# Performance work log

Hardware: AMD Instinct MI355X
Metric: run time of the kernel (lower is better)

## Reference

```python
import jax, jax.numpy as jnp
import numpy as np

EPS = 1e-12  # matches torch F.normalize default eps

def _l2_normalize(x):
    # torch.nn.functional.normalize: x / max(||x||_2, eps)
    n = jnp.sqrt(jnp.sum(x * x, axis=-1, keepdims=True))
    return x / jnp.maximum(n, EPS)

def setup_inputs() -> dict:
    key = jax.random.key(0)
    kq, kk, kv = jax.random.split(key, 3)
    B, N, M, C = 8, 4096, 4096, 256
    return {
        "query": jax.random.normal(kq, (B, N, C), dtype=jnp.float32),
        "key": jax.random.normal(kk, (B, M, C), dtype=jnp.float32),
        "value": jax.random.normal(kv, (B, M, C), dtype=jnp.float32),
    }

def reference(query, key, value):
    B, N, C = query.shape
    q = _l2_normalize(query)          # (B, N, C)
    k = _l2_normalize(key)            # (B, M, C)
    kv = jnp.einsum('bmc,bmd->bcd', k, value)   # (B, C, C)
    context = jnp.einsum('bnc,bcd->bnd', q, kv) # (B, N, C)
    return context / N
```

## Files before the change

### kernel.cpp

```cpp
#include <hip/hip_runtime.h>

typedef __attribute__((ext_vector_type(4))) float v4f;
typedef __attribute__((ext_vector_type(8))) short short8;
typedef unsigned short u16;
typedef unsigned int u32;
typedef __attribute__((ext_vector_type(2))) unsigned int u32x2;
typedef __attribute__((ext_vector_type(4))) unsigned short u16x4;
typedef __attribute__((ext_vector_type(8))) unsigned short u16x8;

#define CDIM 256
#define NB 8
#define NN 4096
#define MM 4096

static __device__ __forceinline__ u16 f2bf(float f) {
  unsigned u = __float_as_uint(f);
  u = (u + 0x7fffu + ((u >> 16) & 1u)) >> 16;
  return (u16)u;
}
static __device__ __forceinline__ float bf2f(u16 h) {
  return __uint_as_float(((unsigned)h) << 16);
}
static __device__ __forceinline__ u32 pack2(float a, float b) {
  return (u32)f2bf(a) | ((u32)f2bf(b) << 16);
}

static __device__ __forceinline__ u32x2 xpose4(u32 A, u32 B, int hi) {
  u32 tA = (u32)__shfl_xor((int)A, 32);
  u32 tB = (u32)__shfl_xor((int)B, 32);
  u32 U = (hi < 2) ? A : tB;
  u32 V = (hi < 2) ? tA : B;
  u32 tU = (u32)__shfl_xor((int)U, 16);
  u32 tV = (u32)__shfl_xor((int)V, 16);
  u32 Up, Vp;
  if ((hi & 1) == 0) {
    Up = (U & 0xffffu) | (tU << 16);
    Vp = (V & 0xffffu) | (tV << 16);
  } else {
    Up = (tU >> 16) | (U & 0xffff0000u);
    Vp = (tV >> 16) | (V & 0xffff0000u);
  }
  return (u32x2){Up, Vp};
}

__global__ __launch_bounds__(512) void kv_kernel(const float* __restrict__ key,
                                                 const float* __restrict__ value,
                                                 u16* __restrict__ partial, int KC) {
  __shared__ __align__(16) u16 knT[2][256 * 64];
  __shared__ __align__(16) u16 vT[2][256 * 64];
  int t = threadIdx.x;
  int b = blockIdx.y, s = blockIdx.x;
  int w = t >> 6, lane = t & 63, lo = lane & 15, hi = lane >> 4;

  const float* kbase = key + ((size_t)b * MM + (size_t)s * KC) * CDIM;
  const float* vbase = value + ((size_t)b * MM + (size_t)s * KC) * CDIM;

  v4f acc[2][16];
  #pragma unroll
  for (int i = 0; i < 2; i++)
    #pragma unroll
    for (int d = 0; d < 16; d++) acc[i][d] = (v4f){0.f, 0.f, 0.f, 0.f};

  v4f kq[4], vq[4];

  auto LOADS = [&](int sc, int it) {
    int row = sc * 64 + w * 8 + it * 4 + hi;
    const float* kr = kbase + (size_t)row * CDIM + lo * 4;
    const float* vr = vbase + (size_t)row * CDIM + lo * 4;
    #pragma unroll
    for (int qt = 0; qt < 4; ++qt) {
      kq[qt] = *(const v4f*)(kr + qt * 64);
      vq[qt] = *(const v4f*)(vr + qt * 64);
    }
  };
  auto STORE = [&](int bufi, int it) {
    int m0 = w * 8 + it * 4;
    float ss = 0.f;
    #pragma unroll
    for (int qt = 0; qt < 4; ++qt)
      ss += kq[qt][0]*kq[qt][0] + kq[qt][1]*kq[qt][1] + kq[qt][2]*kq[qt][2] + kq[qt][3]*kq[qt][3];
    #pragma unroll
    for (int m = 1; m < 16; m <<= 1) ss += __shfl_xor(ss, m);
    float sc_ = 1.0f / fmaxf(sqrtf(ss), 1e-12f);
    #pragma unroll
    for (int qt = 0; qt < 4; ++qt) {
      int c = qt * 64 + lo * 4 + hi;
      int idx = (c * 64 + m0) ^ ((c & 7) << 3);
      u32x2 ko = xpose4(pack2(kq[qt][0] * sc_, kq[qt][1] * sc_),
                        pack2(kq[qt][2] * sc_, kq[qt][3] * sc_), hi);
      *(u32x2*)&knT[bufi][idx] = ko;
      u32x2 vo = xpose4(pack2(vq[qt][0], vq[qt][1]),
                        pack2(vq[qt][2], vq[qt][3]), hi);
      *(u32x2*)&vT[bufi][idx] = vo;
    }
  };
  auto MF = [&](const u16* KB, const u16* VB) {
    #pragma unroll
    for (int kk = 0; kk < 64; kk += 32) {
      int acol = kk + hi * 8;
      int r0 = w * 32 + lo, r1 = w * 32 + 16 + lo;
      short8 a0 = *(const short8*)&KB[(r0 * 64 + acol) ^ ((r0 & 7) << 3)];
      short8 a1 = *(const short8*)&KB[(r1 * 64 + acol) ^ ((r1 & 7) << 3)];
      #pragma unroll
      for (int dt = 0; dt < 16; ++dt) {
        int drow = dt * 16 + lo;
        short8 bb = *(const short8*)&VB[(drow * 64 + acol) ^ ((drow & 7) << 3)];
        acc[0][dt] = __builtin_amdgcn_mfma_f32_16x16x32_bf16(bb, a0, acc[0][dt], 0, 0, 0);
        acc[1][dt] = __builtin_amdgcn_mfma_f32_16x16x32_bf16(bb, a1, acc[1][dt], 0, 0, 0);
      }
    }
  };

  int nsc = KC >> 6;
  LOADS(0, 0); STORE(0, 0);
  LOADS(0, 1); STORE(0, 1);
  __syncthreads();
  for (int sc = 0; sc < nsc; ++sc) {
    int nb = (sc + 1) & 1;
    if (sc + 1 < nsc) LOADS(sc + 1, 0);
    MF(knT[sc & 1], vT[sc & 1]);
    if (sc + 1 < nsc) {
      STORE(nb, 0);
      LOADS(sc + 1, 1);
      STORE(nb, 1);
    }
    __syncthreads();
  }

  size_t base = ((size_t)(s * NB + b)) << 16;
  #pragma unroll
  for (int i = 0; i < 2; i++) {
    int cc = w * 32 + i * 16 + lo;
    #pragma unroll
    for (int dt = 0; dt < 16; ++dt) {
      int dd = dt * 16 + hi * 4;
      #pragma unroll
      for (int r = 0; r < 4; r++)
        partial[base + (size_t)(dd + r) * 256 + cc] = f2bf(acc[i][dt][r]);
    }
  }
}

__global__ __launch_bounds__(256) void red_kernel(const u16* __restrict__ partial,
                                                  u16* __restrict__ kvT, int splits) {
  int j = blockIdx.x * 256 + threadIdx.x;
  int b = j >> 13;
  int e0 = (j & 8191) * 8;
  size_t off = ((size_t)b << 16) + e0;
  const float inv = 1.0f / 4096.0f;
  float sum[8] = {0.f, 0.f, 0.f, 0.f, 0.f, 0.f, 0.f, 0.f};
  for (int s = 0; s < splits; ++s) {
    u16x8 p = *(const u16x8*)&partial[(((size_t)s * NB) << 16) + off];
    #pragma unroll
    for (int x = 0; x < 8; ++x) sum[x] += bf2f(p[x]);
  }
  u16x8 o;
  #pragma unroll
  for (int x = 0; x < 8; ++x) o[x] = f2bf(sum[x] * inv);
  *(u16x8*)&kvT[off] = o;
}

__global__ __launch_bounds__(512) void ctx_kernel(const float* __restrict__ query,
                                                  const u16* __restrict__ kvT,
                                                  float* __restrict__ out) {
  __shared__ __align__(16) u16 qn[2][16 * 256];
  int t = threadIdx.x;
  int b = blockIdx.y;
  int tile0 = blockIdx.x * 4;
  int w = t >> 6, lane = t & 63, lo = lane & 15, hi = lane >> 4;
  int row = t >> 5, l32 = t & 31;
  const float* qbase = query + (size_t)b * NN * CDIM + (size_t)row * CDIM + l32 * 8;

  const float* qr0 = qbase + (size_t)(tile0 * 16) * CDIM;
  v4f x0 = *(const v4f*)qr0;
  v4f x1 = *(const v4f*)(qr0 + 4);

  const u16* kvb = kvT + ((size_t)b << 16);
  short8 Bf[2][8];
  #pragma unroll
  for (int i = 0; i < 2; i++) {
    int dr = (2 * w + i) * 16 + lo;
    #pragma unroll
    for (int kc = 0; kc < 8; kc++)
      Bf[i][kc] = *(const short8*)&kvb[(size_t)dr * 256 + kc * 32 + 8 * hi];
  }

  {
    float ss = x0[0]*x0[0] + x0[1]*x0[1] + x0[2]*x0[2] + x0[3]*x0[3]
             + x1[0]*x1[0] + x1[1]*x1[1] + x1[2]*x1[2] + x1[3]*x1[3];
    #pragma unroll
    for (int m = 1; m < 32; m <<= 1) ss += __shfl_xor(ss, m);
    float sc = 1.0f / fmaxf(sqrtf(ss), 1e-12f);
    u16x8 qb;
    qb[0] = f2bf(x0[0] * sc); qb[1] = f2bf(x0[1] * sc);
    qb[2] = f2bf(x0[2] * sc); qb[3] = f2bf(x0[3] * sc);
    qb[4] = f2bf(x1[0] * sc); qb[5] = f2bf(x1[1] * sc);
    qb[6] = f2bf(x1[2] * sc); qb[7] = f2bf(x1[3] * sc);
    *(u16x8*)&qn[0][(row * 256 + l32 * 8) ^ ((row & 7) << 3)] = qb;
  }

  int cur = 0;
  #pragma unroll
  for (int nt = 0; nt < 4; ++nt) {
    v4f p0, p1;
    if (nt < 3) {
      const float* qr = qbase + (size_t)((tile0 + nt + 1) * 16) * CDIM;
      p0 = *(const v4f*)qr;
      p1 = *(const v4f*)(qr + 4);
    }
    __syncthreads();
    short8 Af[8];
    #pragma unroll
    for (int kc = 0; kc < 8; kc++)
      Af[kc] = *(const short8*)&qn[cur][(lo * 256 + kc * 32 + 8 * hi) ^ ((lo & 7) << 3)];
    v4f acc0 = (v4f){0.f, 0.f, 0.f, 0.f};
    v4f acc1 = (v4f){0.f, 0.f, 0.f, 0.f};
    #pragma unroll
    for (int kc = 0; kc < 8; kc++) {
      acc0 = __builtin_amdgcn_mfma_f32_16x16x32_bf16(Af[kc], Bf[0][kc], acc0, 0, 0, 0);
      acc1 = __builtin_amdgcn_mfma_f32_16x16x32_bf16(Af[kc], Bf[1][kc], acc1, 0, 0, 0);
    }
    int n0 = (tile0 + nt) * 16;
    #pragma unroll
    for (int r = 0; r < 4; r++) {
      size_t ro = (size_t)(b * NN + n0 + 4 * hi + r) * CDIM;
      out[ro + (2 * w) * 16 + lo] = acc0[r];
      out[ro + (2 * w + 1) * 16 + lo] = acc1[r];
    }
    if (nt < 3) {
      float ss = p0[0]*p0[0] + p0[1]*p0[1] + p0[2]*p0[2] + p0[3]*p0[3]
               + p1[0]*p1[0] + p1[1]*p1[1] + p1[2]*p1[2] + p1[3]*p1[3];
      #pragma unroll
      for (int m = 1; m < 32; m <<= 1) ss += __shfl_xor(ss, m);
      float sc = 1.0f / fmaxf(sqrtf(ss), 1e-12f);
      u16x8 qb;
      qb[0] = f2bf(p0[0] * sc); qb[1] = f2bf(p0[1] * sc);
      qb[2] = f2bf(p0[2] * sc); qb[3] = f2bf(p0[3] * sc);
      qb[4] = f2bf(p1[0] * sc); qb[5] = f2bf(p1[1] * sc);
      qb[6] = f2bf(p1[2] * sc); qb[7] = f2bf(p1[3] * sc);
      *(u16x8*)&qn[cur ^ 1][(row * 256 + l32 * 8) ^ ((row & 7) << 3)] = qb;
      cur ^= 1;
    }
  }
}

extern "C" void kernel_launch(void* const* d_in, const int* in_sizes, int n_in,
                              void* d_out, int out_size, void* d_ws, size_t ws_size,
                              hipStream_t stream) {
  const float* q = (const float*)d_in[0];
  const float* k = (const float*)d_in[1];
  const float* v = (const float*)d_in[2];
  float* out = (float*)d_out;

  int splits = 32;
  while (splits > 2) {
    size_t need = ((size_t)splits + 1ull) * 1048576ull;
    if (need <= ws_size) break;
    splits >>= 1;
  }
  u16* partial = (u16*)d_ws;
  u16* kvT = (u16*)((char*)d_ws + (size_t)splits * 1048576ull);

  kv_kernel<<<dim3(splits, NB), dim3(512), 0, stream>>>(k, v, partial, MM / splits);
  red_kernel<<<dim3(256), dim3(256), 0, stream>>>(partial, kvT, splits);
  ctx_kernel<<<dim3(64, NB), dim3(512), 0, stream>>>(q, kvT, out);
}
```

Measured before the change: 56.83 us.

## Double kv_kernel block to 1024 threads and stage partial writes through LDS

The kv_kernel block grows to 16 waves, and work is split over the output d dimension, so each wave holds half the accumulators and loads one 4-row slice per stage instead of two. This raises the number of waves available to hide latency and cuts register pressure per wave. The epilogue now transposes the bf16 accumulators through shared memory in two halves and writes partials with coalesced 16-byte stores, replacing scattered 2-byte global stores. The cost is extra barriers and LDS traffic in the epilogue, and with 64KB of LDS per block occupancy may still be limited.

```diff
diff --git a/kernel.cpp b/kernel.cpp
--- a/kernel.cpp
+++ b/kernel.cpp
@@ -43,28 +43,29 @@
   return (u32x2){Up, Vp};
 }
 
-__global__ __launch_bounds__(512) void kv_kernel(const float* __restrict__ key,
-                                                 const float* __restrict__ value,
-                                                 u16* __restrict__ partial, int KC) {
+__global__ __launch_bounds__(1024, 4) void kv_kernel(const float* __restrict__ key,
+                                                     const float* __restrict__ value,
+                                                     u16* __restrict__ partial, int KC) {
   __shared__ __align__(16) u16 knT[2][256 * 64];
   __shared__ __align__(16) u16 vT[2][256 * 64];
   int t = threadIdx.x;
   int b = blockIdx.y, s = blockIdx.x;
   int w = t >> 6, lane = t & 63, lo = lane & 15, hi = lane >> 4;
+  int wc = w & 7, wd = w >> 3;
 
   const float* kbase = key + ((size_t)b * MM + (size_t)s * KC) * CDIM;
   const float* vbase = value + ((size_t)b * MM + (size_t)s * KC) * CDIM;
 
-  v4f acc[2][16];
+  v4f acc[2][8];
   #pragma unroll
   for (int i = 0; i < 2; i++)
     #pragma unroll
-    for (int d = 0; d < 16; d++) acc[i][d] = (v4f){0.f, 0.f, 0.f, 0.f};
+    for (int d = 0; d < 8; d++) acc[i][d] = (v4f){0.f, 0.f, 0.f, 0.f};
 
   v4f kq[4], vq[4];
 
-  auto LOADS = [&](int sc, int it) {
-    int row = sc * 64 + w * 8 + it * 4 + hi;
+  auto LOADS = [&](int sc) {
+    int row = sc * 64 + w * 4 + hi;
     const float* kr = kbase + (size_t)row * CDIM + lo * 4;
     const float* vr = vbase + (size_t)row * CDIM + lo * 4;
     #pragma unroll
@@ -73,8 +74,8 @@
       vq[qt] = *(const v4f*)(vr + qt * 64);
     }
   };
-  auto STORE = [&](int bufi, int it) {
-    int m0 = w * 8 + it * 4;
+  auto STORE = [&](int bufi) {
+    int m0 = w * 4;
     float ss = 0.f;
     #pragma unroll
     for (int qt = 0; qt < 4; ++qt)
@@ -98,12 +99,12 @@
     #pragma unroll
     for (int kk = 0; kk < 64; kk += 32) {
       int acol = kk + hi * 8;
-      int r0 = w * 32 + lo, r1 = w * 32 + 16 + lo;
+      int r0 = wc * 32 + lo, r1 = wc * 32 + 16 + lo;
       short8 a0 = *(const short8*)&KB[(r0 * 64 + acol) ^ ((r0 & 7) << 3)];
       short8 a1 = *(const short8*)&KB[(r1 * 64 + acol) ^ ((r1 & 7) << 3)];
       #pragma unroll
-      for (int dt = 0; dt < 16; ++dt) {
-        int drow = dt * 16 + lo;
+      for (int dt = 0; dt < 8; ++dt) {
+        int drow = (wd * 8 + dt) * 16 + lo;
         short8 bb = *(const short8*)&VB[(drow * 64 + acol) ^ ((drow & 7) << 3)];
         acc[0][dt] = __builtin_amdgcn_mfma_f32_16x16x32_bf16(bb, a0, acc[0][dt], 0, 0, 0);
         acc[1][dt] = __builtin_amdgcn_mfma_f32_16x16x32_bf16(bb, a1, acc[1][dt], 0, 0, 0);
@@ -112,31 +113,39 @@
   };
 
   int nsc = KC >> 6;
-  LOADS(0, 0); STORE(0, 0);
-  LOADS(0, 1); STORE(0, 1);
+  LOADS(0);
+  STORE(0);
   __syncthreads();
   for (int sc = 0; sc < nsc; ++sc) {
-    int nb = (sc + 1) & 1;
-    if (sc + 1 < nsc) LOADS(sc + 1, 0);
+    if (sc + 1 < nsc) LOADS(sc + 1);
     MF(knT[sc & 1], vT[sc & 1]);
-    if (sc + 1 < nsc) {
-      STORE(nb, 0);
-      LOADS(sc + 1, 1);
-      STORE(nb, 1);
-    }
+    if (sc + 1 < nsc) STORE((sc + 1) & 1);
     __syncthreads();
   }
 
-  size_t base = ((size_t)(s * NB + b)) << 16;
-  #pragma unroll
-  for (int i = 0; i < 2; i++) {
-    int cc = w * 32 + i * 16 + lo;
-    #pragma unroll
-    for (int dt = 0; dt < 16; ++dt) {
-      int dd = dt * 16 + hi * 4;
+  u16* S = &knT[0][0];
+  size_t pbase = ((size_t)(s * NB + b)) << 16;
+  #pragma unroll
+  for (int p = 0; p < 2; ++p) {
+    if (p) __syncthreads();
+    if (wd == p) {
       #pragma unroll
-      for (int r = 0; r < 4; r++)
-        partial[base + (size_t)(dd + r) * 256 + cc] = f2bf(acc[i][dt][r]);
+      for (int i = 0; i < 2; i++) {
+        int c = wc * 32 + i * 16 + lo;
+        #pragma unroll
+        for (int dt = 0; dt < 8; ++dt) {
+          int dl = dt * 16 + hi * 4;
+          #pragma unroll
+          for (int r = 0; r < 4; r++)
+            S[(dl + r) * 256 + c] = f2bf(acc[i][dt][r]);
+        }
+      }
+    }
+    __syncthreads();
+    #pragma unroll
+    for (int j = 0; j < 4; ++j) {
+      int f = j * 8192 + t * 8;
+      *(u16x8*)&partial[pbase + (size_t)p * 32768 + f] = *(const u16x8*)&S[f];
     }
   }
 }
@@ -261,7 +270,7 @@
   u16* partial = (u16*)d_ws;
   u16* kvT = (u16*)((char*)d_ws + (size_t)splits * 1048576ull);
 
-  kv_kernel<<<dim3(splits, NB), dim3(512), 0, stream>>>(k, v, partial, MM / splits);
+  kv_kernel<<<dim3(splits, NB), dim3(1024), 0, stream>>>(k, v, partial, MM / splits);
   red_kernel<<<dim3(256), dim3(256), 0, stream>>>(partial, kvT, splits);
   ctx_kernel<<<dim3(64, NB), dim3(512), 0, stream>>>(q, kvT, out);
 }
```

Result: slower. 65.48 us (+15.2%).

## Shrink kv staging chunks and double-buffer register prefetch with lighter barriers

Applied to the files above, without the earlier changes.

The kv_kernel now stages 32-row chunks instead of 64 in a half-size LDS double buffer, with a new swizzle for the 32-column layout. Two register sets (A/B) let the global loads for the chunk after next be issued while the MFMAs on the current chunk run. The main loop is unrolled by two and uses one custom barrier per chunk: an explicit LDS wait, s_barrier and a scheduling fence. The aim is to hide global load latency better and cut barrier and LDS cost, at the price of more live registers, which may cause spills under the 512-thread launch bound.

```diff
diff --git a/kernel.cpp b/kernel.cpp
--- a/kernel.cpp
+++ b/kernel.cpp
@@ -23,6 +23,10 @@
 }
 static __device__ __forceinline__ u32 pack2(float a, float b) {
   return (u32)f2bf(a) | ((u32)f2bf(b) << 16);
+}
+
+static __device__ __forceinline__ int sidx32(int c, int m) {
+  return (c * 32 + m) ^ (((c >> 1) & 7) << 3);
 }
 
 static __device__ __forceinline__ u32x2 xpose4(u32 A, u32 B, int hi) {
@@ -43,11 +47,17 @@
   return (u32x2){Up, Vp};
 }
 
+#define BARRIER() do { \
+  asm volatile("s_waitcnt lgkmcnt(0)" ::: "memory"); \
+  __builtin_amdgcn_s_barrier(); \
+  __builtin_amdgcn_sched_barrier(0); \
+} while (0)
+
 __global__ __launch_bounds__(512) void kv_kernel(const float* __restrict__ key,
                                                  const float* __restrict__ value,
                                                  u16* __restrict__ partial, int KC) {
-  __shared__ __align__(16) u16 knT[2][256 * 64];
-  __shared__ __align__(16) u16 vT[2][256 * 64];
+  __shared__ __align__(16) u16 KL[2][256 * 32];
+  __shared__ __align__(16) u16 VL[2][256 * 32];
   int t = threadIdx.x;
   int b = blockIdx.y, s = blockIdx.x;
   int w = t >> 6, lane = t & 63, lo = lane & 15, hi = lane >> 4;
@@ -61,10 +71,10 @@
     #pragma unroll
     for (int d = 0; d < 16; d++) acc[i][d] = (v4f){0.f, 0.f, 0.f, 0.f};
 
-  v4f kq[4], vq[4];
-
-  auto LOADS = [&](int sc, int it) {
-    int row = sc * 64 + w * 8 + it * 4 + hi;
+  v4f kqA[4], vqA[4], kqB[4], vqB[4];
+
+  auto LOADS = [&](int sc, v4f (&kq)[4], v4f (&vq)[4]) {
+    int row = sc * 32 + w * 4 + hi;
     const float* kr = kbase + (size_t)row * CDIM + lo * 4;
     const float* vr = vbase + (size_t)row * CDIM + lo * 4;
     #pragma unroll
@@ -73,8 +83,8 @@
       vq[qt] = *(const v4f*)(vr + qt * 64);
     }
   };
-  auto STORE = [&](int bufi, int it) {
-    int m0 = w * 8 + it * 4;
+  auto STORE = [&](int bufi, v4f (&kq)[4], v4f (&vq)[4]) {
+    int m0 = w * 4;
     float ss = 0.f;
     #pragma unroll
     for (int qt = 0; qt < 4; ++qt)
@@ -85,46 +95,48 @@
     #pragma unroll
     for (int qt = 0; qt < 4; ++qt) {
       int c = qt * 64 + lo * 4 + hi;
-      int idx = (c * 64 + m0) ^ ((c & 7) << 3);
+      int idx = sidx32(c, m0);
       u32x2 ko = xpose4(pack2(kq[qt][0] * sc_, kq[qt][1] * sc_),
                         pack2(kq[qt][2] * sc_, kq[qt][3] * sc_), hi);
-      *(u32x2*)&knT[bufi][idx] = ko;
+      *(u32x2*)&KL[bufi][idx] = ko;
       u32x2 vo = xpose4(pack2(vq[qt][0], vq[qt][1]),
                         pack2(vq[qt][2], vq[qt][3]), hi);
-      *(u32x2*)&vT[bufi][idx] = vo;
+      *(u32x2*)&VL[bufi][idx] = vo;
     }
   };
   auto MF = [&](const u16* KB, const u16* VB) {
-    #pragma unroll
-    for (int kk = 0; kk < 64; kk += 32) {
-      int acol = kk + hi * 8;
-      int r0 = w * 32 + lo, r1 = w * 32 + 16 + lo;
-      short8 a0 = *(const short8*)&KB[(r0 * 64 + acol) ^ ((r0 & 7) << 3)];
-      short8 a1 = *(const short8*)&KB[(r1 * 64 + acol) ^ ((r1 & 7) << 3)];
-      #pragma unroll
-      for (int dt = 0; dt < 16; ++dt) {
-        int drow = dt * 16 + lo;
-        short8 bb = *(const short8*)&VB[(drow * 64 + acol) ^ ((drow & 7) << 3)];
-        acc[0][dt] = __builtin_amdgcn_mfma_f32_16x16x32_bf16(bb, a0, acc[0][dt], 0, 0, 0);
-        acc[1][dt] = __builtin_amdgcn_mfma_f32_16x16x32_bf16(bb, a1, acc[1][dt], 0, 0, 0);
+    int acol = hi * 8;
+    int r0 = w * 32 + lo, r1 = w * 32 + 16 + lo;
+    short8 a0 = *(const short8*)&KB[sidx32(r0, 0) ^ 0 ? sidx32(r0, 0) : sidx32(r0, 0)];
+    a0 = *(const short8*)&KB[(r0 * 32 + acol) ^ (((r0 >> 1) & 7) << 3)];
+    short8 a1 = *(const short8*)&KB[(r1 * 32 + acol) ^ (((r1 >> 1) & 7) << 3)];
+    #pragma unroll
+    for (int dt = 0; dt < 16; ++dt) {
+      int drow = dt * 16 + lo;
+      short8 bb = *(const short8*)&VB[(drow * 32 + acol) ^ (((drow >> 1) & 7) << 3)];
+      acc[0][dt] = __builtin_amdgcn_mfma_f32_16x16x32_bf16(bb, a0, acc[0][dt], 0, 0, 0);
+      acc[1][dt] = __builtin_amdgcn_mfma_f32_16x16x32_bf16(bb, a1, acc[1][dt], 0, 0, 0);
+    }
+  };
+
+  int nsc = KC >> 5;
+  LOADS(0, kqA, vqA);
+  LOADS(1, kqB, vqB);
+  STORE(0, kqA, vqA);
+  BARRIER();
+  for (int i = 0; i < nsc; i += 2) {
+    if (i + 2 < nsc) LOADS(i + 2, kqA, vqA);
+    MF(KL[0], VL[0]);
+    if (i + 1 < nsc) {
+      STORE(1, kqB, vqB);
+      BARRIER();
+      if (i + 3 < nsc) LOADS(i + 3, kqB, vqB);
+      MF(KL[1], VL[1]);
+      if (i + 2 < nsc) {
+        STORE(0, kqA, vqA);
+        BARRIER();
       }
     }
-  };
-
-  int nsc = KC >> 6;
-  LOADS(0, 0); STORE(0, 0);
-  LOADS(0, 1); STORE(0, 1);
-  __syncthreads();
-  for (int sc = 0; sc < nsc; ++sc) {
-    int nb = (sc + 1) & 1;
-    if (sc + 1 < nsc) LOADS(sc + 1, 0);
-    MF(knT[sc & 1], vT[sc & 1]);
-    if (sc + 1 < nsc) {
-      STORE(nb, 0);
-      LOADS(sc + 1, 1);
-      STORE(nb, 1);
-    }
-    __syncthreads();
   }
 
   size_t base = ((size_t)(s * NB + b)) << 16;
```

After: 57.78 us. No clear change (+1.7%).

## Split K/V normalize-transpose into separate pre-pass writing bf16 swizzled panels

Applied to the files above, without the earlier changes.

Moves K normalization, bf16 conversion and transposition out of the KV GEMM into a new conv_kernel that writes pre-swizzled 32-row bf16 panels to workspace. The GEMM kernel then copies those panels straight into shared memory and runs MFMAs on 32-wide K chunks with double buffering. This aims to take the conversion and shuffle work off the GEMM's critical path. In exchange it adds an extra launch and a round trip of bf16 panels through global memory.

```diff
diff --git a/kernel.cpp b/kernel.cpp
--- a/kernel.cpp
+++ b/kernel.cpp
@@ -5,13 +5,13 @@
 typedef unsigned short u16;
 typedef unsigned int u32;
 typedef __attribute__((ext_vector_type(2))) unsigned int u32x2;
-typedef __attribute__((ext_vector_type(4))) unsigned short u16x4;
 typedef __attribute__((ext_vector_type(8))) unsigned short u16x8;
 
 #define CDIM 256
 #define NB 8
 #define NN 4096
 #define MM 4096
+#define PANEL 8192
 
 static __device__ __forceinline__ u16 f2bf(float f) {
   unsigned u = __float_as_uint(f);
@@ -23,6 +23,10 @@
 }
 static __device__ __forceinline__ u32 pack2(float a, float b) {
   return (u32)f2bf(a) | ((u32)f2bf(b) << 16);
+}
+
+static __device__ __forceinline__ int sidx32(int c, int m) {
+  return (c * 32 + m) ^ (((c >> 1) & 7) << 3);
 }
 
 static __device__ __forceinline__ u32x2 xpose4(u32 A, u32 B, int hi) {
@@ -43,17 +47,53 @@
   return (u32x2){Up, Vp};
 }
 
-__global__ __launch_bounds__(512) void kv_kernel(const float* __restrict__ key,
-                                                 const float* __restrict__ value,
-                                                 u16* __restrict__ partial, int KC) {
-  __shared__ __align__(16) u16 knT[2][256 * 64];
-  __shared__ __align__(16) u16 vT[2][256 * 64];
+__global__ __launch_bounds__(512) void conv_kernel(const float* __restrict__ key,
+                                                   const float* __restrict__ value,
+                                                   u16* __restrict__ ktp,
+                                                   u16* __restrict__ vtp) {
+  int t = threadIdx.x;
+  int w = t >> 6, lane = t & 63, lo = lane & 15, hi = lane >> 4;
+  int m0 = w * 4;
+  size_t grow = (size_t)blockIdx.x * 32 + m0 + hi;
+  const float* kr = key + grow * CDIM + lo * 4;
+  const float* vr = value + grow * CDIM + lo * 4;
+  v4f kq[4], vq[4];
+  #pragma unroll
+  for (int qt = 0; qt < 4; ++qt) {
+    kq[qt] = *(const v4f*)(kr + qt * 64);
+    vq[qt] = *(const v4f*)(vr + qt * 64);
+  }
+  float ss = 0.f;
+  #pragma unroll
+  for (int qt = 0; qt < 4; ++qt)
+    ss += kq[qt][0]*kq[qt][0] + kq[qt][1]*kq[qt][1] + kq[qt][2]*kq[qt][2] + kq[qt][3]*kq[qt][3];
+  #pragma unroll
+  for (int m = 1; m < 16; m <<= 1) ss += __shfl_xor(ss, m);
+  float sc_ = 1.0f / fmaxf(sqrtf(ss), 1e-12f);
+  u16* kp = ktp + (size_t)blockIdx.x * PANEL;
+  u16* vp = vtp + (size_t)blockIdx.x * PANEL;
+  #pragma unroll
+  for (int qt = 0; qt < 4; ++qt) {
+    int c = qt * 64 + lo * 4 + hi;
+    int idx = sidx32(c, m0);
+    u32x2 ko = xpose4(pack2(kq[qt][0] * sc_, kq[qt][1] * sc_),
+                      pack2(kq[qt][2] * sc_, kq[qt][3] * sc_), hi);
+    *(u32x2*)&kp[idx] = ko;
+    u32x2 vo = xpose4(pack2(vq[qt][0], vq[qt][1]),
+                      pack2(vq[qt][2], vq[qt][3]), hi);
+    *(u32x2*)&vp[idx] = vo;
+  }
+}
+
+__global__ __launch_bounds__(512) void gemm_kernel(const u16* __restrict__ ktp,
+                                                   const u16* __restrict__ vtp,
+                                                   u16* __restrict__ partial, int KC) {
+  __shared__ __align__(16) u16 KL[2][PANEL];
+  __shared__ __align__(16) u16 VL[2][PANEL];
   int t = threadIdx.x;
   int b = blockIdx.y, s = blockIdx.x;
   int w = t >> 6, lane = t & 63, lo = lane & 15, hi = lane >> 4;
-
-  const float* kbase = key + ((size_t)b * MM + (size_t)s * KC) * CDIM;
-  const float* vbase = value + ((size_t)b * MM + (size_t)s * KC) * CDIM;
+  size_t p0 = ((size_t)b * MM + (size_t)s * KC) >> 5;
 
   v4f acc[2][16];
   #pragma unroll
@@ -61,68 +101,50 @@
     #pragma unroll
     for (int d = 0; d < 16; d++) acc[i][d] = (v4f){0.f, 0.f, 0.f, 0.f};
 
-  v4f kq[4], vq[4];
-
-  auto LOADS = [&](int sc, int it) {
-    int row = sc * 64 + w * 8 + it * 4 + hi;
-    const float* kr = kbase + (size_t)row * CDIM + lo * 4;
-    const float* vr = vbase + (size_t)row * CDIM + lo * 4;
-    #pragma unroll
-    for (int qt = 0; qt < 4; ++qt) {
-      kq[qt] = *(const v4f*)(kr + qt * 64);
-      vq[qt] = *(const v4f*)(vr + qt * 64);
+  int soff = t * 16;
+
+  auto MF = [&](const u16* KB, const u16* VB) {
+    int acol = hi * 8;
+    int r0 = w * 32 + lo, r1 = w * 32 + 16 + lo;
+    short8 a0 = *(const short8*)&KB[(r0 * 32 + acol) ^ (((r0 >> 1) & 7) << 3)];
+    short8 a1 = *(const short8*)&KB[(r1 * 32 + acol) ^ (((r1 >> 1) & 7) << 3)];
+    #pragma unroll
+    for (int dt = 0; dt < 16; ++dt) {
+      int drow = dt * 16 + lo;
+      short8 bb = *(const short8*)&VB[(drow * 32 + acol) ^ (((drow >> 1) & 7) << 3)];
+      acc[0][dt] = __builtin_amdgcn_mfma_f32_16x16x32_bf16(bb, a0, acc[0][dt], 0, 0, 0);
+      acc[1][dt] = __builtin_amdgcn_mfma_f32_16x16x32_bf16(bb, a1, acc[1][dt], 0, 0, 0);
     }
   };
-  auto STORE = [&](int bufi, int it) {
-    int m0 = w * 8 + it * 4;
-    float ss = 0.f;
-    #pragma unroll
-    for (int qt = 0; qt < 4; ++qt)
-      ss += kq[qt][0]*kq[qt][0] + kq[qt][1]*kq[qt][1] + kq[qt][2]*kq[qt][2] + kq[qt][3]*kq[qt][3];
-    #pragma unroll
-    for (int m = 1; m < 16; m <<= 1) ss += __shfl_xor(ss, m);
-    float sc_ = 1.0f / fmaxf(sqrtf(ss), 1e-12f);
-    #pragma unroll
-    for (int qt = 0; qt < 4; ++qt) {
-      int c = qt * 64 + lo * 4 + hi;
-      int idx = (c * 64 + m0) ^ ((c & 7) << 3);
-      u32x2 ko = xpose4(pack2(kq[qt][0] * sc_, kq[qt][1] * sc_),
-                        pack2(kq[qt][2] * sc_, kq[qt][3] * sc_), hi);
-      *(u32x2*)&knT[bufi][idx] = ko;
-      u32x2 vo = xpose4(pack2(vq[qt][0], vq[qt][1]),
-                        pack2(vq[qt][2], vq[qt][3]), hi);
-      *(u32x2*)&vT[bufi][idx] = vo;
-    }
-  };
-  auto MF = [&](const u16* KB, const u16* VB) {
-    #pragma unroll
-    for (int kk = 0; kk < 64; kk += 32) {
-      int acol = kk + hi * 8;
-      int r0 = w * 32 + lo, r1 = w * 32 + 16 + lo;
-      short8 a0 = *(const short8*)&KB[(r0 * 64 + acol) ^ ((r0 & 7) << 3)];
-      short8 a1 = *(const short8*)&KB[(r1 * 64 + acol) ^ ((r1 & 7) << 3)];
-      #pragma unroll
-      for (int dt = 0; dt < 16; ++dt) {
-        int drow = dt * 16 + lo;
-        short8 bb = *(const short8*)&VB[(drow * 64 + acol) ^ ((drow & 7) << 3)];
-        acc[0][dt] = __builtin_amdgcn_mfma_f32_16x16x32_bf16(bb, a0, acc[0][dt], 0, 0, 0);
-        acc[1][dt] = __builtin_amdgcn_mfma_f32_16x16x32_bf16(bb, a1, acc[1][dt], 0, 0, 0);
-      }
-    }
-  };
-
-  int nsc = KC >> 6;
-  LOADS(0, 0); STORE(0, 0);
-  LOADS(0, 1); STORE(0, 1);
+
+  int nsc = KC >> 5;
+  {
+    u16x8 k0 = *(const u16x8*)&ktp[p0 * PANEL + soff];
+    u16x8 k1 = *(const u16x8*)&ktp[p0 * PANEL + soff + 8];
+    u16x8 v0 = *(const u16x8*)&vtp[p0 * PANEL + soff];
+    u16x8 v1 = *(const u16x8*)&vtp[p0 * PANEL + soff + 8];
+    *(u16x8*)&KL[0][soff] = k0;
+    *(u16x8*)&KL[0][soff + 8] = k1;
+    *(u16x8*)&VL[0][soff] = v0;
+    *(u16x8*)&VL[0][soff + 8] = v1;
+  }
   __syncthreads();
   for (int sc = 0; sc < nsc; ++sc) {
-    int nb = (sc + 1) & 1;
-    if (sc + 1 < nsc) LOADS(sc + 1, 0);
-    MF(knT[sc & 1], vT[sc & 1]);
+    u16x8 k0N, k1N, v0N, v1N;
     if (sc + 1 < nsc) {
-      STORE(nb, 0);
-      LOADS(sc + 1, 1);
-      STORE(nb, 1);
+      size_t pb = (p0 + sc + 1) * PANEL + soff;
+      k0N = *(const u16x8*)&ktp[pb];
+      k1N = *(const u16x8*)&ktp[pb + 8];
+      v0N = *(const u16x8*)&vtp[pb];
+      v1N = *(const u16x8*)&vtp[pb + 8];
+    }
+    MF(KL[sc & 1], VL[sc & 1]);
+    if (sc + 1 < nsc) {
+      int nb = (sc + 1) & 1;
+      *(u16x8*)&KL[nb][soff] = k0N;
+      *(u16x8*)&KL[nb][soff + 8] = k1N;
+      *(u16x8*)&VL[nb][soff] = v0N;
+      *(u16x8*)&VL[nb][soff + 8] = v1N;
     }
     __syncthreads();
   }
@@ -252,16 +274,20 @@
   const float* v = (const float*)d_in[2];
   float* out = (float*)d_out;
 
+  size_t panels_bytes = 2ull * 1024 * PANEL * 2;
   int splits = 32;
   while (splits > 2) {
-    size_t need = ((size_t)splits + 1ull) * 1048576ull;
+    size_t need = panels_bytes + ((size_t)splits + 1ull) * 1048576ull;
     if (need <= ws_size) break;
     splits >>= 1;
   }
-  u16* partial = (u16*)d_ws;
-  u16* kvT = (u16*)((char*)d_ws + (size_t)splits * 1048576ull);
-
-  kv_kernel<<<dim3(splits, NB), dim3(512), 0, stream>>>(k, v, partial, MM / splits);
+  u16* ktp = (u16*)d_ws;
+  u16* vtp = ktp + (size_t)1024 * PANEL;
+  u16* partial = vtp + (size_t)1024 * PANEL;
+  u16* kvT = partial + (size_t)splits * 524288ull;
+
+  conv_kernel<<<dim3(1024), dim3(512), 0, stream>>>(k, v, ktp, vtp);
+  gemm_kernel<<<dim3(splits, NB), dim3(512), 0, stream>>>(ktp, vtp, partial, MM / splits);
   red_kernel<<<dim3(256), dim3(256), 0, stream>>>(partial, kvT, splits);
   ctx_kernel<<<dim3(64, NB), dim3(512), 0, stream>>>(q, kvT, out);
 }
```

After: 76.90 us. 1.35x slower.
